# Kernel optimization log

Measured on AMD Instinct MI355X. Metric: run time of the kernel, lower is better.

Reference implementation:

```python
import jax, jax.numpy as jnp
import numpy as np

PC_RANGE = (-54.0, -54.0, -5.0, 54.0, 54.0, 3.0)
VOXEL = (0.075, 0.075, 0.2)
STRIDE = 8
FW = 180  # feature map size along x
FH = 180  # feature map size along y
NUM_CLASS = 2
M = 500   # num_max_objs
MIN_RADIUS = 2
OVERLAP = 0.1
C_IN = 128
HM_C = 2
REG_C = 9
B = 4


def conv2d(x, w, b=None):
    y = jax.lax.conv_general_dilated(x, w, (1, 1), 'SAME',
                                     dimension_numbers=('NCHW', 'OIHW', 'NCHW'))
    return y if b is None else y + b[None, :, None, None]


def bn(x, g, b, m, v, eps=1e-5):
    inv = g / jnp.sqrt(v + eps)
    return x * inv[None, :, None, None] + (b - m * inv)[None, :, None, None]


def gaussian_radius(height, width, min_overlap):
    # centernet_utils.gaussian_radius
    b1 = height + width
    c1 = width * height * (1.0 - min_overlap) / (1.0 + min_overlap)
    r1 = (b1 + jnp.sqrt(jnp.maximum(b1 * b1 - 4.0 * c1, 0.0))) / 2.0
    b2 = 2.0 * (height + width)
    c2 = (1.0 - min_overlap) * width * height
    r2 = (b2 + jnp.sqrt(jnp.maximum(b2 * b2 - 16.0 * c2, 0.0))) / 2.0
    a3 = 4.0 * min_overlap
    b3 = -2.0 * min_overlap * (height + width)
    c3 = (min_overlap - 1.0) * width * height
    r3 = (b3 + jnp.sqrt(jnp.maximum(b3 * b3 - 4.0 * a3 * c3, 0.0))) / (2.0 * a3)
    return jnp.minimum(jnp.minimum(r1, r2), r3)


def assign_targets(gt):
    # gt: (B, M, 8) = [x, y, z, dx, dy, dz, ry, cls]; cls==0 / zero box = padding
    x, y, z = gt[..., 0], gt[..., 1], gt[..., 2]
    dx, dy, dz, ry = gt[..., 3], gt[..., 4], gt[..., 5], gt[..., 6]
    cls = gt[..., 7].astype(jnp.int32)
    coord_x = jnp.clip((x - PC_RANGE[0]) / VOXEL[0] / STRIDE, 0.0, FW - 0.5)
    coord_y = jnp.clip((y - PC_RANGE[1]) / VOXEL[1] / STRIDE, 0.0, FH - 0.5)
    cxi = coord_x.astype(jnp.int32)
    cyi = coord_y.astype(jnp.int32)
    dxp = dx / VOXEL[0] / STRIDE
    dyp = dy / VOXEL[1] / STRIDE
    radius = jnp.maximum(gaussian_radius(dxp, dyp, OVERLAP).astype(jnp.int32), MIN_RADIUS)
    valid = (dxp > 0) & (dyp > 0)
    pos = valid & (cls >= 1)

    # --- dense gaussian splat, max-reduced per class (= draw_gaussian_to_heatmap) ---
    ddx = jnp.arange(FW)[None, None, :] - cxi[..., None]   # (B,M,FW)
    ddy = jnp.arange(FH)[None, None, :] - cyi[..., None]   # (B,M,FH)
    sigma = (2.0 * radius.astype(jnp.float32) + 1.0) / 6.0
    d2 = (ddy[..., :, None] ** 2 + ddx[..., None, :] ** 2).astype(jnp.float32)  # (B,M,FH,FW)
    g = jnp.exp(-d2 / (2.0 * sigma[..., None, None] ** 2))
    win = (jnp.abs(ddy) <= radius[..., None])[..., :, None] & \
          (jnp.abs(ddx) <= radius[..., None])[..., None, :]
    g = jnp.where(win & pos[..., None, None], g, 0.0)
    seg = jnp.where(pos, cls - 1, NUM_CLASS)
    hmv = jax.vmap(lambda gv, sv: jax.ops.segment_max(gv, sv, num_segments=NUM_CLASS + 1))(
        g.reshape(B, M, FH * FW), seg)
    heatmap = jnp.maximum(hmv[:, :NUM_CLASS].reshape(B, NUM_CLASS, FH, FW), 0.0)
    heatmap_mask = (heatmap > 0).astype(gt.dtype)

    # --- inds / mask / ret_boxes (5 slots per object: center + 4 neighbors) ---
    base_ind = cyi * FW + cxi
    w_cond = VOXEL[0] * STRIDE > dy / 4.0   # faithful: uses temp_w = gt[:,4]
    l_cond = VOXEL[1] * STRIDE > dx / 4.0   # faithful: uses temp_l = gt[:,3]
    left = cxi - 1 >= 0
    right = cxi + 1 < FW
    up = cyi - 1 >= 0
    down = cyi + 1 < FH
    m0 = jnp.where(valid, jnp.where(cls >= 1, 1, -1), 0)
    s1 = valid & ~w_cond & left
    s2 = valid & ~w_cond & right
    s3 = valid & ~l_cond & up
    s4 = valid & ~l_cond & down
    mask = jnp.stack([m0,
                      jnp.where(s1, m0, 0), jnp.where(s2, m0, 0),
                      jnp.where(s3, m0, 0), jnp.where(s4, m0, 0)], -1).reshape(B, 5 * M)
    inds = jnp.stack([jnp.where(valid, base_ind, 0),
                      jnp.where(s1, base_ind - 1, 0), jnp.where(s2, base_ind + 1, 0),
                      jnp.where(s3, base_ind - FW, 0), jnp.where(s4, base_ind + FW, 0)],
                     -1).reshape(B, 5 * M).astype(jnp.int32)
    offx = coord_x - cxi.astype(gt.dtype)
    offy = coord_y - cyi.astype(gt.dtype)
    base = jnp.stack([offx, offy, z,
                      jnp.log(jnp.maximum(dx, 1e-8)),
                      jnp.log(jnp.maximum(dy, 1e-8)),
                      jnp.log(jnp.maximum(dz, 1e-8)),
                      jnp.cos(ry), jnp.sin(ry)], -1)          # (B,M,8)
    z5 = jnp.zeros((B, M), gt.dtype)
    dx_adj = jnp.stack([z5, s1.astype(gt.dtype), -s2.astype(gt.dtype), z5, z5], -1)  # (B,M,5)
    dy_adj = jnp.stack([z5, z5, z5, s3.astype(gt.dtype), -s4.astype(gt.dtype)], -1)
    zero5 = jnp.zeros_like(dx_adj)
    delta = jnp.stack([dx_adj, dy_adj, zero5, zero5, zero5, zero5, zero5, zero5], -1)  # (B,M,5,8)
    rb = (base[:, :, None, :] + delta) * valid[:, :, None, None].astype(gt.dtype)
    ret_boxes = rb.reshape(B, 5 * M, 8)
    return heatmap, ret_boxes, inds, mask, heatmap_mask


def setup_inputs():
    key = jax.random.key(0)
    ks = jax.random.split(key, 12)
    x = jax.random.normal(ks[0], (B, C_IN, FH, FW), jnp.float32)
    # realistic gt boxes; last 150 per scene are zero padding
    cxy = jax.random.uniform(ks[1], (B, M, 2), minval=-50.0, maxval=50.0)
    zc = jax.random.uniform(ks[2], (B, M, 1), minval=-2.0, maxval=1.0)
    dims = jax.random.uniform(ks[3], (B, M, 3), minval=0.5, maxval=6.0)
    ry = jax.random.uniform(ks[4], (B, M, 1), minval=-3.14, maxval=3.14)
    cls = jax.random.randint(ks[5], (B, M, 1), 1, NUM_CLASS + 1).astype(jnp.float32)
    vm = (jnp.arange(M) < 350)[None, :, None].astype(jnp.float32)
    gt_boxes = jnp.concatenate([cxy, zc, dims, ry, cls], -1) * vm
    p = lambda k, s, sc: jax.random.normal(k, s, jnp.float32) * sc
    return {
        'x': x, 'gt_boxes': gt_boxes,
        'conv1_w': p(ks[6], (C_IN, C_IN, 3, 3), 0.02),
        'bn1_g': jnp.ones((C_IN,)), 'bn1_b': jnp.zeros((C_IN,)),
        'bn1_m': jnp.zeros((C_IN,)), 'bn1_v': jnp.ones((C_IN,)),
        'conv2_w': p(ks[7], (C_IN, C_IN, 3, 3), 0.02),
        'bn2_g': jnp.ones((C_IN,)), 'bn2_b': jnp.zeros((C_IN,)),
        'bn2_m': jnp.zeros((C_IN,)), 'bn2_v': jnp.ones((C_IN,)),
        'hm_w': p(ks[8], (HM_C, C_IN, 3, 3), 0.02),
        'hm_b': jnp.full((HM_C,), -2.19, jnp.float32),
        'reg_w': p(ks[9], (REG_C, C_IN, 3, 3), 0.001),
        'reg_b': jnp.zeros((REG_C,), jnp.float32),
    }


def reference(x, gt_boxes, conv1_w, bn1_g, bn1_b, bn1_m, bn1_v,
              conv2_w, bn2_g, bn2_b, bn2_m, bn2_v, hm_w, hm_b, reg_w, reg_b):
    f = jax.nn.relu(bn(conv2d(x, conv1_w), bn1_g, bn1_b, bn1_m, bn1_v))
    f = jax.nn.relu(bn(conv2d(f, conv2_w), bn2_g, bn2_b, bn2_m, bn2_v))
    hm = conv2d(f, hm_w, hm_b)      # (B, 2, H, W)
    reg = conv2d(f, reg_w, reg_b)   # (B, 9, H, W)
    heatmap, ret_boxes, inds, mask, heatmap_mask = assign_targets(gt_boxes)
    return hm, reg, heatmap, ret_boxes, inds, mask, heatmap_mask
```

## Files before the change

### kernel.cpp

```cpp
#include <hip/hip_runtime.h>
#include <math.h>

typedef unsigned short u16;
typedef short bf16x8 __attribute__((ext_vector_type(8)));
typedef float f32x4 __attribute__((ext_vector_type(4)));

#define FW_ 180
#define FH_ 180
#define HW_ (FW_*FH_)
#define CIN_ 128
#define BB_ 4
#define MM_ 500
#define PW_ 182
#define PADE ((size_t)BB_*PW_*PW_*CIN_)

#define HM_OFF   0
#define REG_OFF  (BB_*2*HW_)
#define HEAT_OFF (REG_OFF + BB_*9*HW_)
#define RB_OFF   (HEAT_OFF + BB_*2*HW_)
#define IND_OFF  (RB_OFF + BB_*MM_*5*8)
#define MSK_OFF  (IND_OFF + BB_*MM_*5)
#define HMM_OFF  (MSK_OFF + BB_*MM_*5)

__device__ inline u16 f2bf(float f) {
    unsigned u = __float_as_uint(f);
    u += 0x7FFFu + ((u >> 16) & 1u);
    return (u16)(u >> 16);
}

#define GLOAD_LDS16(gsrc, ldst) \
    __builtin_amdgcn_global_load_lds( \
        (const __attribute__((address_space(1))) unsigned*)(gsrc), \
        (__attribute__((address_space(3))) unsigned*)(ldst), 16, 0, 0)

__global__ void k_init(u16* __restrict__ ws, float* __restrict__ out)
{
    int idx = blockIdx.x * 256 + threadIdx.x;
    const int n1 = 3 * BB_ * PW_ * PW_;
    if (idx < n1) {
        int buf = idx / (BB_ * PW_ * PW_);
        int rem = idx % (BB_ * PW_ * PW_);
        int p = rem % (PW_ * PW_);
        int r = p / PW_, c = p % PW_;
        if (r > 0 && r < PW_ - 1 && c > 0 && c < PW_ - 1) return;
        u16* base = ws + (size_t)buf * PADE + (size_t)rem * CIN_;
#pragma unroll
        for (int i = 0; i < 16; ++i) ((uint4*)base)[i] = make_uint4(0, 0, 0, 0);
    } else {
        int i = idx - n1;
        if (i < BB_ * 2 * HW_) out[HEAT_OFF + i] = 0.f;
    }
}

__global__ __launch_bounds__(256) void k_prep_xT(const float* __restrict__ in,
                                                 u16* __restrict__ xT)
{
    __shared__ unsigned lt32[180 * 65];
    int tid = threadIdx.x;
    int row = blockIdx.x, b = blockIdx.y;
    const float* inr = in + ((size_t)b * CIN_ * FH_ + row) * FW_;
    for (int i = tid; i < 64 * 45; i += 256) {
        int ci2 = i / 45, c4 = i - 45 * ci2;
        const float* p0 = inr + (size_t)(2 * ci2) * HW_ + c4 * 4;
        float4 a = *(const float4*)p0;
        float4 bq = *(const float4*)(p0 + HW_);
        lt32[(c4 * 4 + 0) * 65 + ci2] = (unsigned)f2bf(a.x) | ((unsigned)f2bf(bq.x) << 16);
        lt32[(c4 * 4 + 1) * 65 + ci2] = (unsigned)f2bf(a.y) | ((unsigned)f2bf(bq.y) << 16);
        lt32[(c4 * 4 + 2) * 65 + ci2] = (unsigned)f2bf(a.z) | ((unsigned)f2bf(bq.z) << 16);
        lt32[(c4 * 4 + 3) * 65 + ci2] = (unsigned)f2bf(a.w) | ((unsigned)f2bf(bq.w) << 16);
    }
    __syncthreads();
    unsigned* dst = (unsigned*)(xT + ((size_t)b * PW_ * PW_ + (size_t)(row + 1) * PW_ + 1) * CIN_);
    for (int idx = tid; idx < 180 * 64; idx += 256) {
        int col = idx >> 6, c2 = idx & 63;
        dst[col * 64 + c2] = lt32[col * 65 + c2];
    }
}

__global__ void k_prep_w(const float* __restrict__ w1, const float* __restrict__ w2,
                         const float* __restrict__ hw, const float* __restrict__ rw,
                         u16* __restrict__ wT1, u16* __restrict__ wT2,
                         u16* __restrict__ wTh)
{
    int i = blockIdx.x * 256 + threadIdx.x;
    const int NW = 9 * CIN_ * CIN_;
    if (i < NW) {
        int tap = i / (CIN_ * CIN_);
        int r = i % (CIN_ * CIN_);
        int co = r >> 7, ci = r & 127;
        wT1[i] = f2bf(w1[((size_t)co * CIN_ + ci) * 9 + tap]);
    } else if (i < 2 * NW) {
        int j = i - NW;
        int tap = j / (CIN_ * CIN_);
        int r = j % (CIN_ * CIN_);
        int co = r >> 7, ci = r & 127;
        wT2[j] = f2bf(w2[((size_t)co * CIN_ + ci) * 9 + tap]);
    } else {
        int j = i - 2 * NW;
        if (j >= 9 * 16 * CIN_) return;
        int tap = j / (16 * CIN_);
        int r = j % (16 * CIN_);
        int co = r >> 7, ci = r & 127;
        float v = 0.f;
        if (co < 2)       v = hw[((size_t)co * CIN_ + ci) * 9 + tap];
        else if (co < 11) v = rw[((size_t)(co - 2) * CIN_ + ci) * 9 + tap];
        wTh[j] = f2bf(v);
    }
}

__global__ __launch_bounds__(256) void k_conv_v5(
    const u16* __restrict__ xT, const u16* __restrict__ wT,
    const float* __restrict__ gg, const float* __restrict__ bbn,
    const float* __restrict__ mmn, const float* __restrict__ vvn,
    u16* __restrict__ yT)
{
    __shared__ u16 lin[1600 * 8];
    __shared__ u16 lwt[2304 * 8];

    int tid  = threadIdx.x;
    int wv   = tid >> 6, lane = tid & 63;
    int lm   = lane & 15, hi = lane >> 4;
    int csp  = blockIdx.x % 3, cog = blockIdx.x / 3;
    int C0   = (csp == 2) ? 116 : csp * 64;
    int cob  = cog * 64;
    int R0   = blockIdx.y * 4;
    int b    = blockIdx.z;
    const u16* xb = xT + (size_t)b * PW_ * PW_ * CIN_;

    f32x4 acc[4][4];
#pragma unroll
    for (int i = 0; i < 4; ++i)
#pragma unroll
        for (int j = 0; j < 4; ++j) acc[i][j] = (f32x4){0.f, 0.f, 0.f, 0.f};

    const int wco = (tid & 255) >> 2;
    const int wq  = (tid & 3) ^ ((wco >> 1) & 3);

#pragma unroll 1
    for (int ch = 0; ch < 4; ++ch) {
        int ci0 = ch * 32;
        __syncthreads();
#pragma unroll
        for (int rd = 0; rd < 6; ++rd) {
            int o = rd * 256 + tid;
            int rc = o >> 2;
            int r = rc / 66, c = rc - 66 * r;
            int q = (o & 3) ^ ((c >> 1) & 3);
            const u16* src = xb + ((size_t)(R0 + r) * PW_ + (C0 + c)) * CIN_ + ci0 + q * 8;
            GLOAD_LDS16(src, &lin[(size_t)(rd * 256 + wv * 64) * 8]);
        }
        if (wv == 0) {
            int o = 1536 + lane;
            int rc = o >> 2;
            int r = rc / 66, c = rc - 66 * r;
            if (o >= 1584) { r = 5; c = 65; }
            int q = (o & 3) ^ ((c >> 1) & 3);
            const u16* src = xb + ((size_t)(R0 + r) * PW_ + (C0 + c)) * CIN_ + ci0 + q * 8;
            GLOAD_LDS16(src, &lin[(size_t)1536 * 8]);
        }
#pragma unroll
        for (int tap = 0; tap < 9; ++tap) {
            const u16* src = wT + (size_t)tap * CIN_ * CIN_ + (size_t)(cob + wco) * CIN_ + ci0 + wq * 8;
            GLOAD_LDS16(src, &lwt[(size_t)(tap * 256 + wv * 64) * 8]);
        }
        __syncthreads();

#pragma unroll
        for (int tap = 0; tap < 9; ++tap) {
            const int kr = tap / 3, kc = tap - 3 * (tap / 3);
            bf16x8 av[4];
#pragma unroll
            for (int mf = 0; mf < 4; ++mf) {
                int col = mf * 16 + lm;
                int unit = tap * 256 + col * 4 + (hi ^ ((col >> 1) & 3));
                av[mf] = *(const bf16x8*)&lwt[(size_t)unit * 8];
            }
#pragma unroll
            for (int nf = 0; nf < 4; ++nf) {
                int c = wv * 16 + lm + kc;
                int rc = (nf + kr) * 66 + c;
                int unit = rc * 4 + (hi ^ ((c >> 1) & 3));
                bf16x8 bv = *(const bf16x8*)&lin[(size_t)unit * 8];
#pragma unroll
                for (int mf = 0; mf < 4; ++mf)
                    acc[mf][nf] = __builtin_amdgcn_mfma_f32_16x16x32_bf16(
                        av[mf], bv, acc[mf][nf], 0, 0, 0);
            }
        }
    }

#pragma unroll
    for (int mf = 0; mf < 4; ++mf) {
        int co0 = cob + mf * 16 + hi * 4;
        float4 g4 = *(const float4*)(gg + co0);
        float4 b4 = *(const float4*)(bbn + co0);
        float4 m4 = *(const float4*)(mmn + co0);
        float4 v4 = *(const float4*)(vvn + co0);
        float sc0 = g4.x / sqrtf(v4.x + 1e-5f), sh0 = b4.x - m4.x * sc0;
        float sc1 = g4.y / sqrtf(v4.y + 1e-5f), sh1 = b4.y - m4.y * sc1;
        float sc2 = g4.z / sqrtf(v4.z + 1e-5f), sh2 = b4.z - m4.z * sc2;
        float sc3 = g4.w / sqrtf(v4.w + 1e-5f), sh3 = b4.w - m4.w * sc3;
#pragma unroll
        for (int nf = 0; nf < 4; ++nf) {
            f32x4 A = acc[mf][nf];
            float y0 = fmaxf(fmaf(A[0], sc0, sh0), 0.f);
            float y1 = fmaxf(fmaf(A[1], sc1, sh1), 0.f);
            float y2 = fmaxf(fmaf(A[2], sc2, sh2), 0.f);
            float y3 = fmaxf(fmaf(A[3], sc3, sh3), 0.f);
            unsigned p0 = (unsigned)f2bf(y0) | ((unsigned)f2bf(y1) << 16);
            unsigned p1 = (unsigned)f2bf(y2) | ((unsigned)f2bf(y3) << 16);
            u16* op = yT + (size_t)b * PW_ * PW_ * CIN_ +
                      ((size_t)(R0 + nf + 1) * PW_ + (C0 + wv * 16 + lm + 1)) * CIN_ + co0;
            *(uint2*)op = make_uint2(p0, p1);
        }
    }
}

__global__ __launch_bounds__(256) void k_head_v5(
    const u16* __restrict__ f2T, const u16* __restrict__ wTh,
    const float* __restrict__ hb, const float* __restrict__ rb,
    float* __restrict__ out)
{
    __shared__ u16 lin[1600 * 8];
    __shared__ u16 lwt[2304 * 8];

    int tid  = threadIdx.x;
    int wv   = tid >> 6, lane = tid & 63;
    int lm   = lane & 15, hi = lane >> 4;
    int csp  = blockIdx.x;
    int C0   = (csp == 2) ? 116 : csp * 64;
    int R0   = blockIdx.y * 4;
    int b    = blockIdx.z;
    const u16* xb = f2T + (size_t)b * PW_ * PW_ * CIN_;

    f32x4 acc[4];
#pragma unroll
    for (int i = 0; i < 4; ++i) acc[i] = (f32x4){0.f, 0.f, 0.f, 0.f};

#pragma unroll
    for (int rd = 0; rd < 9; ++rd) {
        int o = rd * 256 + tid;
        int tap = o >> 8, rest = o & 255;
        int co = rest >> 4, u8s = rest & 15;
        const u16* src = wTh + (size_t)tap * 16 * CIN_ + co * CIN_ + ((u8s ^ (co & 7)) * 8);
        GLOAD_LDS16(src, &lwt[(size_t)(rd * 256 + wv * 64) * 8]);
    }

#pragma unroll 1
    for (int ch = 0; ch < 4; ++ch) {
        int ci0 = ch * 32;
        __syncthreads();
#pragma unroll
        for (int rd = 0; rd < 6; ++rd) {
            int o = rd * 256 + tid;
            int rc = o >> 2;
            int r = rc / 66, c = rc - 66 * r;
            int q = (o & 3) ^ ((c >> 1) & 3);
            const u16* src = xb + ((size_t)(R0 + r) * PW_ + (C0 + c)) * CIN_ + ci0 + q * 8;
            GLOAD_LDS16(src, &lin[(size_t)(rd * 256 + wv * 64) * 8]);
        }
        if (wv == 0) {
            int o = 1536 + lane;
            int rc = o >> 2;
            int r = rc / 66, c = rc - 66 * r;
            if (o >= 1584) { r = 5; c = 65; }
            int q = (o & 3) ^ ((c >> 1) & 3);
            const u16* src = xb + ((size_t)(R0 + r) * PW_ + (C0 + c)) * CIN_ + ci0 + q * 8;
            GLOAD_LDS16(src, &lin[(size_t)1536 * 8]);
        }
        __syncthreads();

#pragma unroll
        for (int tap = 0; tap < 9; ++tap) {
            const int kr = tap / 3, kc = tap - 3 * (tap / 3);
            int u8 = (ch * 4 + hi) ^ (lm & 7);
            bf16x8 av = *(const bf16x8*)&lwt[(size_t)(tap * 256 + lm * 16 + u8) * 8];
#pragma unroll
            for (int nf = 0; nf < 4; ++nf) {
                int c = wv * 16 + lm + kc;
                int rc = (nf + kr) * 66 + c;
                int unit = rc * 4 + (hi ^ ((c >> 1) & 3));
                bf16x8 bv = *(const bf16x8*)&lin[(size_t)unit * 8];
                acc[nf] = __builtin_amdgcn_mfma_f32_16x16x32_bf16(av, bv, acc[nf], 0, 0, 0);
            }
        }
    }

#pragma unroll
    for (int nf = 0; nf < 4; ++nf) {
        int row = R0 + nf, col = C0 + wv * 16 + lm;
        f32x4 A = acc[nf];
#pragma unroll
        for (int r = 0; r < 4; ++r) {
            int co = hi * 4 + r;
            float v = A[r];
            if (co < 2)
                out[HM_OFF + ((size_t)(b * 2 + co)) * HW_ + (size_t)row * FW_ + col] = v + hb[co];
            else if (co < 11)
                out[REG_OFF + ((size_t)(b * 9 + co - 2)) * HW_ + (size_t)row * FW_ + col] = v + rb[co - 2];
        }
    }
}

__global__ void k_objects(const float* __restrict__ gt, float* __restrict__ out)
{
    int ob = blockIdx.x;
    int b = ob / MM_, m = ob % MM_;
    const float* gp = gt + (size_t)ob * 8;
    float x = gp[0], y = gp[1], z = gp[2];
    float dx = gp[3], dy = gp[4], dz = gp[5], ry = gp[6];
    int cls = (int)gp[7];

    float coord_x = fminf(fmaxf((x + 54.f) / 0.075f / 8.f, 0.f), 179.5f);
    float coord_y = fminf(fmaxf((y + 54.f) / 0.075f / 8.f, 0.f), 179.5f);
    int cxi = (int)coord_x, cyi = (int)coord_y;
    float dxp = dx / 0.075f / 8.f;
    float dyp = dy / 0.075f / 8.f;

    float hgt = dxp, wid = dyp, mo = 0.1f;
    float b1 = hgt + wid, c1 = wid * hgt * (1.f - mo) / (1.f + mo);
    float r1 = (b1 + sqrtf(fmaxf(b1 * b1 - 4.f * c1, 0.f))) * 0.5f;
    float b2 = 2.f * (hgt + wid), c2 = (1.f - mo) * wid * hgt;
    float r2 = (b2 + sqrtf(fmaxf(b2 * b2 - 16.f * c2, 0.f))) * 0.5f;
    float a3 = 4.f * mo, b3 = -2.f * mo * (hgt + wid), c3 = (mo - 1.f) * wid * hgt;
    float r3 = (b3 + sqrtf(fmaxf(b3 * b3 - 4.f * a3 * c3, 0.f))) / (2.f * a3);
    int radius = max((int)fminf(fminf(r1, r2), r3), 2);

    bool valid = (dxp > 0.f) && (dyp > 0.f);
    bool pos = valid && (cls >= 1);

    if (threadIdx.x == 0) {
        float m0 = valid ? (cls >= 1 ? 1.f : -1.f) : 0.f;
        bool w_cond = (0.075f * 8.f) > dy / 4.f;
        bool l_cond = (0.075f * 8.f) > dx / 4.f;
        bool s1 = valid && !w_cond && (cxi - 1 >= 0);
        bool s2 = valid && !w_cond && (cxi + 1 < FW_);
        bool s3 = valid && !l_cond && (cyi - 1 >= 0);
        bool s4 = valid && !l_cond && (cyi + 1 < FH_);
        int base_ind = cyi * FW_ + cxi;

        float* indp = out + IND_OFF + (size_t)b * MM_ * 5 + m * 5;
        float* mskp = out + MSK_OFF + (size_t)b * MM_ * 5 + m * 5;
        indp[0] = valid ? (float)base_ind : 0.f;
        indp[1] = s1 ? (float)(base_ind - 1) : 0.f;
        indp[2] = s2 ? (float)(base_ind + 1) : 0.f;
        indp[3] = s3 ? (float)(base_ind - FW_) : 0.f;
        indp[4] = s4 ? (float)(base_ind + FW_) : 0.f;
        mskp[0] = m0;
        mskp[1] = s1 ? m0 : 0.f;
        mskp[2] = s2 ? m0 : 0.f;
        mskp[3] = s3 ? m0 : 0.f;
        mskp[4] = s4 ? m0 : 0.f;

        float offx = coord_x - (float)cxi;
        float offy = coord_y - (float)cyi;
        float bse[8] = { offx, offy, z,
                         logf(fmaxf(dx, 1e-8f)), logf(fmaxf(dy, 1e-8f)),
                         logf(fmaxf(dz, 1e-8f)), cosf(ry), sinf(ry) };
        float vm = valid ? 1.f : 0.f;
        float* rbp = out + RB_OFF + ((size_t)b * MM_ + m) * 5 * 8;
#pragma unroll
        for (int s = 0; s < 5; ++s) {
            float t0 = bse[0], t1 = bse[1];
            if (s == 1) t0 += s1 ? 1.f : 0.f;
            if (s == 2) t0 -= s2 ? 1.f : 0.f;
            if (s == 3) t1 += s3 ? 1.f : 0.f;
            if (s == 4) t1 -= s4 ? 1.f : 0.f;
            rbp[s * 8 + 0] = t0 * vm;
            rbp[s * 8 + 1] = t1 * vm;
#pragma unroll
            for (int k = 2; k < 8; ++k) rbp[s * 8 + k] = bse[k] * vm;
        }
    }

    if (pos) {
        float sigma = (2.f * (float)radius + 1.f) / 6.f;
        float inv2s2 = 1.f / (2.f * sigma * sigma);
        int x0 = max(cxi - radius, 0), x1 = min(cxi + radius, FW_ - 1);
        int y0 = max(cyi - radius, 0), y1 = min(cyi + radius, FH_ - 1);
        int wdt = x1 - x0 + 1, tot = wdt * (y1 - y0 + 1);
        float* hp = out + HEAT_OFF + (size_t)(b * 2 + (cls - 1)) * HW_;
        for (int i = threadIdx.x; i < tot; i += blockDim.x) {
            int yy = y0 + i / wdt, xx = x0 + i % wdt;
            float ddy = (float)(yy - cyi), ddx = (float)(xx - cxi);
            float gvl = expf(-(ddy * ddy + ddx * ddx) * inv2s2);
            atomicMax((int*)(hp + yy * FW_ + xx), __float_as_int(gvl));
        }
    }
}

__global__ void k_hm_mask(float* __restrict__ out)
{
    int i = blockIdx.x * 256 + threadIdx.x;
    if (i < BB_ * 2 * HW_) {
        float v = out[HEAT_OFF + i];
        out[HMM_OFF + i] = v > 0.f ? 1.f : 0.f;
    }
}

extern "C" void kernel_launch(void* const* d_in, const int* in_sizes, int n_in,
                              void* d_out, int out_size, void* d_ws, size_t ws_size,
                              hipStream_t stream)
{
    const float* x  = (const float*)d_in[0];
    const float* gt = (const float*)d_in[1];
    const float* w1 = (const float*)d_in[2];
    const float* g1 = (const float*)d_in[3];
    const float* b1 = (const float*)d_in[4];
    const float* m1 = (const float*)d_in[5];
    const float* v1 = (const float*)d_in[6];
    const float* w2 = (const float*)d_in[7];
    const float* g2 = (const float*)d_in[8];
    const float* b2 = (const float*)d_in[9];
    const float* m2 = (const float*)d_in[10];
    const float* v2 = (const float*)d_in[11];
    const float* hw = (const float*)d_in[12];
    const float* hb = (const float*)d_in[13];
    const float* rw = (const float*)d_in[14];
    const float* rb = (const float*)d_in[15];
    float* out = (float*)d_out;

    u16* ws  = (u16*)d_ws;
    u16* xT  = ws;
    u16* f1T = ws + PADE;
    u16* f2T = ws + 2 * PADE;
    u16* wT1 = ws + 3 * PADE;
    u16* wT2 = wT1 + 9 * CIN_ * CIN_;
    u16* wTh = wT2 + 9 * CIN_ * CIN_;

    const int NINIT = 3 * BB_ * PW_ * PW_ + BB_ * 2 * HW_;
    k_init<<<(NINIT + 255) / 256, 256, 0, stream>>>(ws, out);
    k_prep_xT<<<dim3(180, BB_), 256, 0, stream>>>(x, xT);
    const int NWALL = 2 * 9 * CIN_ * CIN_ + 9 * 16 * CIN_;
    k_prep_w<<<(NWALL + 255) / 256, 256, 0, stream>>>(w1, w2, hw, rw, wT1, wT2, wTh);

    dim3 cg(6, 45, BB_);
    k_conv_v5<<<cg, 256, 0, stream>>>(xT,  wT1, g1, b1, m1, v1, f1T);
    k_conv_v5<<<cg, 256, 0, stream>>>(f1T, wT2, g2, b2, m2, v2, f2T);

    dim3 hg(3, 45, BB_);
    k_head_v5<<<hg, 256, 0, stream>>>(f2T, wTh, hb, rb, out);

    k_objects<<<BB_ * MM_, 64, 0, stream>>>(gt, out);
    k_hm_mask<<<(BB_ * 2 * HW_ + 255) / 256, 256, 0, stream>>>(out);
}
```

Baseline: 158.3 us.

## Fuse prep kernels, read conv weights directly from global, fold mask into head

Merges the weight transpose into the init kernel and folds the heatmap-mask pass into the head kernel, cutting two launches. The object kernel now runs before the convolutions. The conv kernel drops its LDS weight stage and loads A fragments straight from global/L2. It also precomputes the input-tile source offsets and requests 4 blocks per CU through launch bounds. The xT transpose store is widened to 16-byte writes. Dropping the weight LDS buffer lowers LDS use and may raise occupancy, at the cost of more global load latency inside the MFMA loop.

```diff
diff --git a/kernel.cpp b/kernel.cpp
--- a/kernel.cpp
+++ b/kernel.cpp
@@ -33,10 +33,19 @@
         (const __attribute__((address_space(1))) unsigned*)(gsrc), \
         (__attribute__((address_space(3))) unsigned*)(ldst), 16, 0, 0)
 
-__global__ void k_init(u16* __restrict__ ws, float* __restrict__ out)
+__global__ void k_init_w(u16* __restrict__ ws, float* __restrict__ out,
+                         const float* __restrict__ w1, const float* __restrict__ w2,
+                         const float* __restrict__ hw, const float* __restrict__ rw,
+                         u16* __restrict__ wT1, u16* __restrict__ wT2,
+                         u16* __restrict__ wTh)
 {
     int idx = blockIdx.x * 256 + threadIdx.x;
     const int n1 = 3 * BB_ * PW_ * PW_;
+    const int n2 = n1 + BB_ * 2 * HW_;
+    const int NW = 9 * CIN_ * CIN_;
+    const int n3 = n2 + NW;
+    const int n4 = n3 + NW;
+    const int n5 = n4 + 9 * 16 * CIN_;
     if (idx < n1) {
         int buf = idx / (BB_ * PW_ * PW_);
         int rem = idx % (BB_ * PW_ * PW_);
@@ -46,9 +55,29 @@
         u16* base = ws + (size_t)buf * PADE + (size_t)rem * CIN_;
 #pragma unroll
         for (int i = 0; i < 16; ++i) ((uint4*)base)[i] = make_uint4(0, 0, 0, 0);
-    } else {
-        int i = idx - n1;
-        if (i < BB_ * 2 * HW_) out[HEAT_OFF + i] = 0.f;
+    } else if (idx < n2) {
+        out[HEAT_OFF + (idx - n1)] = 0.f;
+    } else if (idx < n3) {
+        int j = idx - n2;
+        int tap = j / (CIN_ * CIN_);
+        int r = j % (CIN_ * CIN_);
+        int co = r >> 7, ci = r & 127;
+        wT1[j] = f2bf(w1[((size_t)co * CIN_ + ci) * 9 + tap]);
+    } else if (idx < n4) {
+        int j = idx - n3;
+        int tap = j / (CIN_ * CIN_);
+        int r = j % (CIN_ * CIN_);
+        int co = r >> 7, ci = r & 127;
+        wT2[j] = f2bf(w2[((size_t)co * CIN_ + ci) * 9 + tap]);
+    } else if (idx < n5) {
+        int j = idx - n4;
+        int tap = j / (16 * CIN_);
+        int r = j % (16 * CIN_);
+        int co = r >> 7, ci = r & 127;
+        float v = 0.f;
+        if (co < 2)       v = hw[((size_t)co * CIN_ + ci) * 9 + tap];
+        else if (co < 11) v = rw[((size_t)(co - 2) * CIN_ + ci) * 9 + tap];
+        wTh[j] = f2bf(v);
     }
 }
 
@@ -71,51 +100,24 @@
     }
     __syncthreads();
     unsigned* dst = (unsigned*)(xT + ((size_t)b * PW_ * PW_ + (size_t)(row + 1) * PW_ + 1) * CIN_);
-    for (int idx = tid; idx < 180 * 64; idx += 256) {
-        int col = idx >> 6, c2 = idx & 63;
-        dst[col * 64 + c2] = lt32[col * 65 + c2];
-    }
-}
-
-__global__ void k_prep_w(const float* __restrict__ w1, const float* __restrict__ w2,
-                         const float* __restrict__ hw, const float* __restrict__ rw,
-                         u16* __restrict__ wT1, u16* __restrict__ wT2,
-                         u16* __restrict__ wTh)
-{
-    int i = blockIdx.x * 256 + threadIdx.x;
-    const int NW = 9 * CIN_ * CIN_;
-    if (i < NW) {
-        int tap = i / (CIN_ * CIN_);
-        int r = i % (CIN_ * CIN_);
-        int co = r >> 7, ci = r & 127;
-        wT1[i] = f2bf(w1[((size_t)co * CIN_ + ci) * 9 + tap]);
-    } else if (i < 2 * NW) {
-        int j = i - NW;
-        int tap = j / (CIN_ * CIN_);
-        int r = j % (CIN_ * CIN_);
-        int co = r >> 7, ci = r & 127;
-        wT2[j] = f2bf(w2[((size_t)co * CIN_ + ci) * 9 + tap]);
-    } else {
-        int j = i - 2 * NW;
-        if (j >= 9 * 16 * CIN_) return;
-        int tap = j / (16 * CIN_);
-        int r = j % (16 * CIN_);
-        int co = r >> 7, ci = r & 127;
-        float v = 0.f;
-        if (co < 2)       v = hw[((size_t)co * CIN_ + ci) * 9 + tap];
-        else if (co < 11) v = rw[((size_t)(co - 2) * CIN_ + ci) * 9 + tap];
-        wTh[j] = f2bf(v);
-    }
-}
-
-__global__ __launch_bounds__(256) void k_conv_v5(
+    for (int idx = tid; idx < 180 * 16; idx += 256) {
+        int col = idx >> 4, q = idx & 15;
+        uint4 v;
+        v.x = lt32[col * 65 + q * 4 + 0];
+        v.y = lt32[col * 65 + q * 4 + 1];
+        v.z = lt32[col * 65 + q * 4 + 2];
+        v.w = lt32[col * 65 + q * 4 + 3];
+        *(uint4*)&dst[col * 64 + q * 4] = v;
+    }
+}
+
+__global__ __launch_bounds__(256, 4) void k_conv_v9(
     const u16* __restrict__ xT, const u16* __restrict__ wT,
     const float* __restrict__ gg, const float* __restrict__ bbn,
     const float* __restrict__ mmn, const float* __restrict__ vvn,
     u16* __restrict__ yT)
 {
     __shared__ u16 lin[1600 * 8];
-    __shared__ u16 lwt[2304 * 8];
 
     int tid  = threadIdx.x;
     int wv   = tid >> 6, lane = tid & 63;
@@ -133,36 +135,36 @@
 #pragma unroll
         for (int j = 0; j < 4; ++j) acc[i][j] = (f32x4){0.f, 0.f, 0.f, 0.f};
 
-    const int wco = (tid & 255) >> 2;
-    const int wq  = (tid & 3) ^ ((wco >> 1) & 3);
+    unsigned soffI[6];
+#pragma unroll
+    for (int rd = 0; rd < 6; ++rd) {
+        int o = rd * 256 + tid;
+        int rc = o >> 2;
+        int r = rc / 66, c = rc - 66 * r;
+        int q = (o & 3) ^ ((c >> 1) & 3);
+        soffI[rd] = (unsigned)(((R0 + r) * PW_ + (C0 + c)) * CIN_ + q * 8);
+    }
+    unsigned soffX = 0;
+    if (tid < 64) {
+        int o = 1536 + tid;
+        int rc = o >> 2;
+        int r = rc / 66, c = rc - 66 * r;
+        if (o >= 1584) { r = 5; c = 65; }
+        int q = (o & 3) ^ ((c >> 1) & 3);
+        soffX = (unsigned)(((R0 + r) * PW_ + (C0 + c)) * CIN_ + q * 8);
+    }
+
+    const u16* aB = wT + (size_t)(cob + lm) * CIN_ + hi * 8;
 
 #pragma unroll 1
     for (int ch = 0; ch < 4; ++ch) {
-        int ci0 = ch * 32;
+        const int ci0 = ch * 32;
         __syncthreads();
 #pragma unroll
-        for (int rd = 0; rd < 6; ++rd) {
-            int o = rd * 256 + tid;
-            int rc = o >> 2;
-            int r = rc / 66, c = rc - 66 * r;
-            int q = (o & 3) ^ ((c >> 1) & 3);
-            const u16* src = xb + ((size_t)(R0 + r) * PW_ + (C0 + c)) * CIN_ + ci0 + q * 8;
-            GLOAD_LDS16(src, &lin[(size_t)(rd * 256 + wv * 64) * 8]);
-        }
-        if (wv == 0) {
-            int o = 1536 + lane;
-            int rc = o >> 2;
-            int r = rc / 66, c = rc - 66 * r;
-            if (o >= 1584) { r = 5; c = 65; }
-            int q = (o & 3) ^ ((c >> 1) & 3);
-            const u16* src = xb + ((size_t)(R0 + r) * PW_ + (C0 + c)) * CIN_ + ci0 + q * 8;
-            GLOAD_LDS16(src, &lin[(size_t)1536 * 8]);
-        }
-#pragma unroll
-        for (int tap = 0; tap < 9; ++tap) {
-            const u16* src = wT + (size_t)tap * CIN_ * CIN_ + (size_t)(cob + wco) * CIN_ + ci0 + wq * 8;
-            GLOAD_LDS16(src, &lwt[(size_t)(tap * 256 + wv * 64) * 8]);
-        }
+        for (int rd = 0; rd < 6; ++rd)
+            GLOAD_LDS16(xb + soffI[rd] + ci0, &lin[(size_t)(rd * 256 + wv * 64) * 8]);
+        if (tid < 64)
+            GLOAD_LDS16(xb + soffX + ci0, &lin[(size_t)1536 * 8]);
         __syncthreads();
 
 #pragma unroll
@@ -170,11 +172,8 @@
             const int kr = tap / 3, kc = tap - 3 * (tap / 3);
             bf16x8 av[4];
 #pragma unroll
-            for (int mf = 0; mf < 4; ++mf) {
-                int col = mf * 16 + lm;
-                int unit = tap * 256 + col * 4 + (hi ^ ((col >> 1) & 3));
-                av[mf] = *(const bf16x8*)&lwt[(size_t)unit * 8];
-            }
+            for (int mf = 0; mf < 4; ++mf)
+                av[mf] = *(const bf16x8*)(aB + (size_t)tap * CIN_ * CIN_ + mf * 16 * CIN_ + ci0);
 #pragma unroll
             for (int nf = 0; nf < 4; ++nf) {
                 int c = wv * 16 + lm + kc;
@@ -216,7 +215,7 @@
     }
 }
 
-__global__ __launch_bounds__(256) void k_head_v5(
+__global__ __launch_bounds__(256) void k_head_v9(
     const u16* __restrict__ f2T, const u16* __restrict__ wTh,
     const float* __restrict__ hb, const float* __restrict__ rb,
     float* __restrict__ out)
@@ -259,8 +258,8 @@
             const u16* src = xb + ((size_t)(R0 + r) * PW_ + (C0 + c)) * CIN_ + ci0 + q * 8;
             GLOAD_LDS16(src, &lin[(size_t)(rd * 256 + wv * 64) * 8]);
         }
-        if (wv == 0) {
-            int o = 1536 + lane;
+        if (tid < 64) {
+            int o = 1536 + tid;
             int rc = o >> 2;
             int r = rc / 66, c = rc - 66 * r;
             if (o >= 1584) { r = 5; c = 65; }
@@ -299,6 +298,13 @@
             else if (co < 11)
                 out[REG_OFF + ((size_t)(b * 9 + co - 2)) * HW_ + (size_t)row * FW_ + col] = v + rb[co - 2];
         }
+    }
+
+    int blk = (b * 45 + (int)blockIdx.y) * 3 + csp;
+    int base = blk * 480;
+    for (int i = base + tid; i < base + 480; i += 256) {
+        float v = out[HEAT_OFF + i];
+        out[HMM_OFF + i] = v > 0.f ? 1.f : 0.f;
     }
 }
 
@@ -386,15 +392,6 @@
             float gvl = expf(-(ddy * ddy + ddx * ddx) * inv2s2);
             atomicMax((int*)(hp + yy * FW_ + xx), __float_as_int(gvl));
         }
-    }
-}
-
-__global__ void k_hm_mask(float* __restrict__ out)
-{
-    int i = blockIdx.x * 256 + threadIdx.x;
-    if (i < BB_ * 2 * HW_) {
-        float v = out[HEAT_OFF + i];
-        out[HMM_OFF + i] = v > 0.f ? 1.f : 0.f;
     }
 }
 
@@ -428,19 +425,17 @@
     u16* wT2 = wT1 + 9 * CIN_ * CIN_;
     u16* wTh = wT2 + 9 * CIN_ * CIN_;
 
-    const int NINIT = 3 * BB_ * PW_ * PW_ + BB_ * 2 * HW_;
-    k_init<<<(NINIT + 255) / 256, 256, 0, stream>>>(ws, out);
+    const int NTOT = 3 * BB_ * PW_ * PW_ + BB_ * 2 * HW_
+                   + 2 * 9 * CIN_ * CIN_ + 9 * 16 * CIN_;
+    k_init_w<<<(NTOT + 255) / 256, 256, 0, stream>>>(ws, out, w1, w2, hw, rw,
+                                                     wT1, wT2, wTh);
     k_prep_xT<<<dim3(180, BB_), 256, 0, stream>>>(x, xT);
-    const int NWALL = 2 * 9 * CIN_ * CIN_ + 9 * 16 * CIN_;
-    k_prep_w<<<(NWALL + 255) / 256, 256, 0, stream>>>(w1, w2, hw, rw, wT1, wT2, wTh);
+    k_objects<<<BB_ * MM_, 64, 0, stream>>>(gt, out);
 
     dim3 cg(6, 45, BB_);
-    k_conv_v5<<<cg, 256, 0, stream>>>(xT,  wT1, g1, b1, m1, v1, f1T);
-    k_conv_v5<<<cg, 256, 0, stream>>>(f1T, wT2, g2, b2, m2, v2, f2T);
+    k_conv_v9<<<cg, 256, 0, stream>>>(xT,  wT1, g1, b1, m1, v1, f1T);
+    k_conv_v9<<<cg, 256, 0, stream>>>(f1T, wT2, g2, b2, m2, v2, f2T);
 
     dim3 hg(3, 45, BB_);
-    k_head_v5<<<hg, 256, 0, stream>>>(f2T, wTh, hb, rb, out);
-
-    k_objects<<<BB_ * MM_, 64, 0, stream>>>(gt, out);
-    k_hm_mask<<<(BB_ * 2 * HW_ + 255) / 256, 256, 0, stream>>>(out);
-}
+    k_head_v9<<<hg, 256, 0, stream>>>(f2T, wTh, hb, rb, out);
+}
```

Measured after the change: 325.5 us. 2.06x slower.
